# Optimization experiments

Hardware: AMD Instinct MI355X
Metric: run time of the kernel (lower is better)

## Reference

```python
import jax, jax.numpy as jnp
import numpy as np
from jax import lax

B, T = 32, 20
H, E, A, V = 256, 512, 256, 10000
GH, GW, D = 32, 32, 256          # info spatial grid and channel dim
P = GH * GW                      # num_pixels = 1024
IN_FLAT = P * D                  # 262144
REL = 128 * 128                  # 16384
LSTM_IN = E + D + H              # input to gate linears (x = [word, att_feat], then cat h)


def setup_inputs() -> dict:
    key = jax.random.key(0)
    ks = iter(jax.random.split(key, 40))
    def W(shape, scale=0.05):
        return jax.random.normal(next(ks), shape, jnp.float32) * scale
    inp = {}
    inp["info"] = jax.random.normal(next(ks), (B, GH, GW, D), jnp.float32)
    inp["relation"] = jax.random.normal(next(ks), (B, 128, 128), jnp.float32)
    inp["captions"] = jax.random.randint(next(ks), (B, T), 0, V)
    lens = jax.random.randint(next(ks), (B, 1), 5, T + 1).at[0, 0].set(T)
    inp["captions_lens"] = lens
    # embedding + attention
    inp["emb"] = W((V, E), 0.1)
    inp["W_enc"] = W((D, A)); inp["b_enc"] = jnp.zeros((A,), jnp.float32)
    inp["W_dec"] = W((H, A)); inp["b_dec"] = jnp.zeros((A,), jnp.float32)
    inp["W_full"] = W((A,));  inp["b_full"] = jnp.zeros((), jnp.float32)
    # MSLSTM cell (5 gate linears + mlp)
    for g in ("i", "f", "o", "g1", "g2"):
        inp[f"W_{g}"] = W((LSTM_IN, H)); inp[f"b_{g}"] = jnp.zeros((H,), jnp.float32)
    inp["W_mlp"] = W((2 * H, H)); inp["b_mlp"] = jnp.zeros((H,), jnp.float32)
    # f_beta, fc, init-state linears
    inp["W_beta"] = W((H, D)); inp["b_beta"] = jnp.zeros((D,), jnp.float32)
    inp["W_fc"] = W((H, V), 0.1); inp["b_fc"] = jnp.zeros((V,), jnp.float32)
    inp["W_ih"] = W((IN_FLAT, H), 0.005); inp["b_ih"] = jnp.zeros((H,), jnp.float32)
    inp["W_ic"] = W((IN_FLAT, H), 0.005); inp["b_ic"] = jnp.zeros((H,), jnp.float32)
    inp["W_iC"] = W((REL, H), 0.01);      inp["b_iC"] = jnp.zeros((H,), jnp.float32)
    return inp


def reference(info, relation, captions, captions_lens, emb,
              W_enc, b_enc, W_dec, b_dec, W_full, b_full,
              W_i, b_i, W_f, b_f, W_o, b_o, W_g1, b_g1, W_g2, b_g2,
              W_mlp, b_mlp, W_beta, b_beta, W_fc, b_fc,
              W_ih, b_ih, W_ic, b_ic, W_iC, b_iC):
    Bsz = captions.shape[0]
    info_f = info.reshape(Bsz, P, D)
    rel_f = relation.reshape(Bsz, REL)
    lens = captions_lens[:, 0]
    order = jnp.argsort(-lens)                      # sort descending by length
    lens = lens[order]
    caps = captions[order]
    info_f = info_f[order]
    rel_f = rel_f[order]
    sent_len = lens - 1
    Tm = captions.shape[1] - 1                      # static: max len forced to T in setup

    words = emb[caps]                               # (B, T, E)
    flat = info_f.reshape(Bsz, -1)                  # (B, P*D)
    h = flat @ W_ih + b_ih
    c = flat @ W_ic + b_ic
    C = rel_f @ W_iC + b_iC
    att1 = info_f @ W_enc + b_enc                   # (B, P, A) -- invariant over t

    def step(carry, xs):
        h, c, C = carry
        word, t = xs                                # word: (B, E)
        att2 = h @ W_dec + b_dec                    # (B, A)
        e = jax.nn.relu(att1 + att2[:, None, :]) @ W_full + b_full   # (B, P)
        alpha = jax.nn.softmax(e, axis=1)
        awf = jnp.einsum('bpd,bp->bd', info_f, alpha)                # (B, D)
        # note: gate=sigmoid(f_beta(h)) is computed in torch but its product is unused
        x = jnp.concatenate([word, awf, h], axis=1)  # cat([x, h]) with x=[word, awf]
        i = jax.nn.sigmoid(x @ W_i + b_i)
        f = jax.nn.sigmoid(x @ W_f + b_f)
        o = jax.nn.sigmoid(x @ W_o + b_o)
        g1 = jnp.tanh(x @ W_g1 + b_g1)
        g2 = jnp.tanh(x @ W_g2 + b_g2)
        new_c = f * c + i * g1
        new_C = f * C + i * g2
        new_h = o * jnp.tanh(jnp.concatenate([new_c, new_C], axis=1) @ W_mlp + b_mlp)
        pred = new_h @ W_fc + b_fc                  # dropout in eval mode = identity
        mask = (sent_len > t)[:, None].astype(pred.dtype)
        return (new_h, new_c, new_C), (pred * mask, alpha * mask)

    words_t = jnp.swapaxes(words[:, :Tm], 0, 1)     # (Tm, B, E)
    (_, (preds, alphas)) = lax.scan(step, (h, c, C), (words_t, jnp.arange(Tm)))
    predictions = jnp.swapaxes(preds, 0, 1)         # (B, Tm, V)
    alphas = jnp.swapaxes(alphas, 0, 1)             # (B, Tm, P)
    return predictions, alphas, order
```

## Files before the change

kernel.cpp:

```cpp
#include <hip/hip_runtime.h>
#include <math.h>

#define Bz 32
#define Tz 20
#define TMz 19
#define Vz 10000
#define INFLAT 262144
#define RELSZ 16384
#define NBLK 512

#define WS_PH     0
#define WS_PC     4194304
#define WS_ATT1H  0
#define WS_INFOH  4194304
#define WS_EXPE   8388608
#define WS_ZPART  8421376
#define WS_AWF    8421888
#define WS_GSP    8430080
#define WS_HST    8593920
#define WS_CST0   8602112
#define WS_CSTB0  8610304
#define WS_CST1   8618496
#define WS_CSTB1  8626688
#define WS_AT2P   8634880
#define WS_INTS   8700416
#define WS_PCHC   8701440

__device__ __forceinline__ float sigm(float x) { return 1.0f / (1.0f + expf(-x)); }

__device__ __forceinline__ unsigned short f2bf(float f) {
    unsigned int x = __float_as_uint(f);
    unsigned int r = (x + 0x7fffu + ((x >> 16) & 1u)) >> 16;
    return (unsigned short)r;
}

__device__ __forceinline__ float agload(const float* p) {
    return __hip_atomic_load(p, __ATOMIC_RELAXED, __HIP_MEMORY_SCOPE_AGENT);
}
__device__ __forceinline__ void agstore(float* p, float v) {
    __hip_atomic_store(p, v, __ATOMIC_RELAXED, __HIP_MEMORY_SCOPE_AGENT);
}
__device__ __forceinline__ int agloadi(const int* p) {
    return __hip_atomic_load(p, __ATOMIC_RELAXED, __HIP_MEMORY_SCOPE_AGENT);
}
__device__ __forceinline__ void agstorei(int* p, int v) {
    __hip_atomic_store(p, v, __ATOMIC_RELAXED, __HIP_MEMORY_SCOPE_AGENT);
}
__device__ __forceinline__ void agadd(float* p, float v) {
    __hip_atomic_fetch_add(p, v, __ATOMIC_RELAXED, __HIP_MEMORY_SCOPE_AGENT);
}

__device__ __forceinline__ void gl_lds16(const float* g, float* l) {
    __builtin_amdgcn_global_load_lds(
        (const __attribute__((address_space(1))) unsigned int*)g,
        (__attribute__((address_space(3))) unsigned int*)l,
        16, 0, 0);
}

__device__ __forceinline__ void gbar(int* slots, int* root, int gen) {
    asm volatile("s_waitcnt vmcnt(0)" ::: "memory");
    __syncthreads();
    if (blockIdx.x == 0) {
        int i0 = threadIdx.x, i1 = threadIdx.x + 256;
        if (i0 != 0) {
            while (agloadi(&slots[i0]) < gen) __builtin_amdgcn_s_sleep(1);
        }
        while (agloadi(&slots[i1]) < gen) __builtin_amdgcn_s_sleep(1);
        __syncthreads();
        if (threadIdx.x == 0) agstorei(root, gen);
    } else if (threadIdx.x == 0) {
        agstorei(&slots[blockIdx.x], gen);
        while (agloadi(root) < gen) __builtin_amdgcn_s_sleep(2);
    }
    __syncthreads();
    asm volatile("" ::: "memory");
}

__global__ void k_sort(const int* __restrict__ lens, float* __restrict__ out_order,
                       int* __restrict__ ord, int* __restrict__ sentlen, int* __restrict__ barmem) {
    if (threadIdx.x == 0 && blockIdx.x == 0) {
        for (int i = 0; i < 64 + NBLK; ++i) barmem[i] = 0;
        int l[Bz]; bool used[Bz];
        for (int b = 0; b < Bz; ++b) { l[b] = lens[b]; used[b] = false; }
        for (int i = 0; i < Bz; ++i) {
            int best = -1;
            for (int j = 0; j < Bz; ++j)
                if (!used[j] && (best < 0 || l[j] > l[best])) best = j;
            used[best] = true;
            ord[i] = best;
            sentlen[i] = l[best] - 1;
            out_order[i] = (float)best;
        }
    }
}

__global__ __launch_bounds__(256) void k_gemv2(const float* __restrict__ X, const int* __restrict__ ord,
                                               const float* __restrict__ W1, const float* __restrict__ W2,
                                               float* __restrict__ p1, float* __restrict__ p2) {
    __shared__ __align__(16) float wlds[8192];
    __shared__ __align__(16) float xsT[256 * 36];
    __shared__ int ords[32];
    int tid = threadIdx.x;
    int wv = tid >> 6, ln = tid & 63;
    size_t k0 = (size_t)blockIdx.x * 512;

    if (tid < 32) ords[tid] = ord[tid];
    __syncthreads();

    auto stage_xs = [&](int hh) {
        for (int idx = tid; idx < 2048; idx += 256) {
            int b = idx >> 6, kq = idx & 63;
            float4 v = *(const float4*)&X[(size_t)ords[b] * INFLAT + k0 + (size_t)hh * 256 + kq * 4];
            xsT[(kq * 4 + 0) * 36 + b] = v.x;
            xsT[(kq * 4 + 1) * 36 + b] = v.y;
            xsT[(kq * 4 + 2) * 36 + b] = v.z;
            xsT[(kq * 4 + 3) * 36 + b] = v.w;
        }
    };
    auto issue = [&](int n) {
        int slot = n & 1;
        size_t krow = k0 + (size_t)n * 8 + wv * 2;
        const float* g1 = W1 + krow * 256 + ln * 4;
        const float* g2 = W2 + krow * 256 + ln * 4;
        float* l1 = &wlds[slot * 4096 + (wv * 2) * 256 + ln * 4];
        float* l2 = &wlds[slot * 4096 + 2048 + (wv * 2) * 256 + ln * 4];
        gl_lds16(g1, l1);
        gl_lds16(g2, l2);
        gl_lds16(g1 + 256, l1 + 256);
        gl_lds16(g2 + 256, l2 + 256);
    };

    float ah[32], ac[32];
#pragma unroll
    for (int b = 0; b < 32; ++b) { ah[b] = 0.f; ac[b] = 0.f; }

    stage_xs(0);
    issue(0);

#pragma unroll 1
    for (int c = 0; c < 64; ++c) {
        if (c == 32) stage_xs(1);
        if (c + 1 < 64) {
            issue(c + 1);
            asm volatile("s_waitcnt vmcnt(4)" ::: "memory");
        } else {
            asm volatile("s_waitcnt vmcnt(0)" ::: "memory");
        }
        __syncthreads();
        int slot = c & 1;
        int xb0 = (c & 31) * 8;
#pragma unroll
        for (int kk = 0; kk < 8; ++kk) {
            float w1 = wlds[slot * 4096 + kk * 256 + tid];
            float w2 = wlds[slot * 4096 + 2048 + kk * 256 + tid];
            const float4* xr = (const float4*)&xsT[(xb0 + kk) * 36];
#pragma unroll
            for (int bq = 0; bq < 8; ++bq) {
                float4 x4 = xr[bq];
                ah[bq * 4 + 0] += x4.x * w1; ac[bq * 4 + 0] += x4.x * w2;
                ah[bq * 4 + 1] += x4.y * w1; ac[bq * 4 + 1] += x4.y * w2;
                ah[bq * 4 + 2] += x4.z * w1; ac[bq * 4 + 2] += x4.z * w2;
                ah[bq * 4 + 3] += x4.w * w1; ac[bq * 4 + 3] += x4.w * w2;
            }
        }
        __syncthreads();
    }
#pragma unroll
    for (int b = 0; b < 32; ++b) {
        size_t o = ((size_t)blockIdx.x * 32 + b) * 256 + tid;
        p1[o] = ah[b];
        p2[o] = ac[b];
    }
}

__global__ __launch_bounds__(256) void k_gemvC(const float* __restrict__ R, const int* __restrict__ ord,
                                               const float* __restrict__ W, float* __restrict__ p) {
    __shared__ float xs[32 * 128];
    __shared__ int ords[32];
    int tid = threadIdx.x, bx = blockIdx.x;
    if (tid < 32) ords[tid] = ord[tid];
    __syncthreads();
    int k0 = bx * 128;
    for (int idx = tid; idx < 32 * 128; idx += 256) {
        int b = idx >> 7, kk = idx & 127;
        xs[idx] = R[(size_t)ords[b] * RELSZ + k0 + kk];
    }
    __syncthreads();
    float acc[32];
#pragma unroll
    for (int b = 0; b < 32; ++b) acc[b] = 0.f;
    for (int kk = 0; kk < 128; ++kk) {
        float w = W[(size_t)(k0 + kk) * 256 + tid];
#pragma unroll
        for (int b = 0; b < 32; ++b) acc[b] += xs[b * 128 + kk] * w;
    }
#pragma unroll
    for (int b = 0; b < 32; ++b) p[((size_t)bx * 32 + b) * 256 + tid] = acc[b];
}

__global__ __launch_bounds__(256) void k_reduce3(const float* __restrict__ ph, const float* __restrict__ pc,
                                                 const float* __restrict__ pC,
                                                 const float* __restrict__ b_ih, const float* __restrict__ b_ic,
                                                 const float* __restrict__ b_iC,
                                                 float* __restrict__ hst, float* __restrict__ cst,
                                                 float* __restrict__ Cst) {
    int which = blockIdx.x >> 5, b = blockIdx.x & 31, j = threadIdx.x;
    if (which == 0) {
        float s0 = b_ih[j], s1 = 0.f, s2 = 0.f, s3 = 0.f;
        for (int c = 0; c < 512; c += 4) {
            s0 += ph[((size_t)((c + 0) * 32 + b)) * 256 + j];
            s1 += ph[((size_t)((c + 1) * 32 + b)) * 256 + j];
            s2 += ph[((size_t)((c + 2) * 32 + b)) * 256 + j];
            s3 += ph[((size_t)((c + 3) * 32 + b)) * 256 + j];
        }
        hst[b * 256 + j] = s0 + s1 + s2 + s3;
    } else if (which == 1) {
        float s0 = b_ic[j], s1 = 0.f, s2 = 0.f, s3 = 0.f;
        for (int c = 0; c < 512; c += 4) {
            s0 += pc[((size_t)((c + 0) * 32 + b)) * 256 + j];
            s1 += pc[((size_t)((c + 1) * 32 + b)) * 256 + j];
            s2 += pc[((size_t)((c + 2) * 32 + b)) * 256 + j];
            s3 += pc[((size_t)((c + 3) * 32 + b)) * 256 + j];
        }
        cst[b * 256 + j] = s0 + s1 + s2 + s3;
    } else {
        float s0 = b_iC[j], s1 = 0.f, s2 = 0.f, s3 = 0.f;
        for (int c = 0; c < 128; c += 4) {
            s0 += pC[((size_t)((c + 0) * 32 + b)) * 256 + j];
            s1 += pC[((size_t)((c + 1) * 32 + b)) * 256 + j];
            s2 += pC[((size_t)((c + 2) * 32 + b)) * 256 + j];
            s3 += pC[((size_t)((c + 3) * 32 + b)) * 256 + j];
        }
        Cst[b * 256 + j] = s0 + s1 + s2 + s3;
    }
}

__global__ __launch_bounds__(256) void k_init2(const float* __restrict__ hst, const float* __restrict__ W_dec,
                                               float* __restrict__ at2p, float* __restrict__ awf) {
    __shared__ __align__(16) float hs[8192];
    int tid = threadIdx.x;
    for (int i = blockIdx.x * 256 + tid; i < 8192; i += 1024) awf[i] = 0.f;
    for (int i = tid; i < 2048; i += 256) ((float4*)hs)[i] = ((const float4*)hst)[i];
    __syncthreads();
    int col = blockIdx.x * 64 + (tid & 63), bg = tid >> 6;
    float acc[8] = {0.f,0.f,0.f,0.f,0.f,0.f,0.f,0.f};
    for (int k = 0; k < 256; ++k) {
        float w = W_dec[(size_t)k * 256 + col];
#pragma unroll
        for (int bi = 0; bi < 8; ++bi) acc[bi] += hs[(bg * 8 + bi) * 256 + k] * w;
    }
#pragma unroll
    for (int bi = 0; bi < 8; ++bi) {
        int b = bg * 8 + bi;
        at2p[((size_t)(b * 8 + 0)) * 256 + col] = acc[bi];
#pragma unroll
        for (int ct = 1; ct < 8; ++ct) at2p[((size_t)(b * 8 + ct)) * 256 + col] = 0.f;
    }
}

__global__ __launch_bounds__(256) void k_att1(const float* __restrict__ info, const int* __restrict__ ord,
                                              const float* __restrict__ W, const float* __restrict__ bias,
                                              unsigned short* __restrict__ att1h,
                                              unsigned short* __restrict__ infoh) {
    __shared__ __align__(16) float xsT[256 * 36];
    int tid = threadIdx.x;
    int r0 = blockIdx.x * 32;
    int b = r0 >> 10, p0 = r0 & 1023;
    const float* src = info + (size_t)ord[b] * INFLAT + (size_t)p0 * 256;
    for (int idx = tid; idx < 2048; idx += 256) {
        int r = idx >> 6, kq = idx & 63;
        float4 v = *(const float4*)&src[r * 256 + kq * 4];
        xsT[(kq * 4 + 0) * 36 + r] = v.x;
        xsT[(kq * 4 + 1) * 36 + r] = v.y;
        xsT[(kq * 4 + 2) * 36 + r] = v.z;
        xsT[(kq * 4 + 3) * 36 + r] = v.w;
    }
    __syncthreads();
#pragma unroll 4
    for (int r = 0; r < 32; ++r)
        infoh[(size_t)(r0 + r) * 256 + tid] = f2bf(xsT[tid * 36 + r]);
    float acc[32];
#pragma unroll
    for (int r = 0; r < 32; ++r) acc[r] = 0.f;
    for (int k = 0; k < 256; ++k) {
        float w = W[k * 256 + tid];
        const float4* xr = (const float4*)&xsT[k * 36];
#pragma unroll
        for (int rq = 0; rq < 8; ++rq) {
            float4 x4 = xr[rq];
            acc[rq * 4 + 0] += x4.x * w;
            acc[rq * 4 + 1] += x4.y * w;
            acc[rq * 4 + 2] += x4.z * w;
            acc[rq * 4 + 3] += x4.w * w;
        }
    }
    float bj = bias[tid];
#pragma unroll
    for (int r = 0; r < 32; ++r)
        att1h[(size_t)(r0 + r) * 256 + tid] = f2bf(acc[r] + bj);
}

struct KArgs {
    const float *info, *emb, *W_dec, *b_dec, *W_full, *b_full;
    const float *W_i, *W_f, *W_o, *W_g1, *W_g2;
    const float *b_i, *b_f, *b_o, *b_g1, *b_g2;
    const float *W_mlp, *b_mlp, *W_fc, *b_fc;
    const int *caps;
    const unsigned short *att1h, *infoh;
    float *expe, *zpart, *awf, *gsp, *hst, *cst0, *Cst0, *cst1, *Cst1, *at2p;
    const int *ord, *slp;
    int *root, *slots;
    float *out_pred, *out_alpha;
};

__device__ void pred_task2(const KArgs& a, float* sm, int tile, int tm1) {
    int tid = threadIdx.x;
    for (int i = tid; i < 8192; i += 256) sm[i] = agload(&a.hst[i]);
    __syncthreads();
    int col = tile * 64 + (tid & 63), bg = tid >> 6;
    if (col >= Vz) return;
    float acc[8] = {0.f, 0.f, 0.f, 0.f, 0.f, 0.f, 0.f, 0.f};
    for (int jq = 0; jq < 64; ++jq) {
        float w0 = a.W_fc[(size_t)(jq * 4 + 0) * Vz + col];
        float w1 = a.W_fc[(size_t)(jq * 4 + 1) * Vz + col];
        float w2 = a.W_fc[(size_t)(jq * 4 + 2) * Vz + col];
        float w3 = a.W_fc[(size_t)(jq * 4 + 3) * Vz + col];
#pragma unroll
        for (int bi = 0; bi < 8; ++bi) {
            float4 h4 = *(const float4*)&sm[(bg * 8 + bi) * 256 + jq * 4];
            acc[bi] += h4.x * w0 + h4.y * w1 + h4.z * w2 + h4.w * w3;
        }
    }
    float bv = a.b_fc[col];
#pragma unroll
    for (int bi = 0; bi < 8; ++bi) {
        int b = bg * 8 + bi;
        float r = (a.slp[b] > tm1) ? (acc[bi] + bv) : 0.f;
        a.out_pred[((size_t)b * TMz + tm1) * Vz + col] = r;
    }
}

__global__ __launch_bounds__(256, 2) void k_steps(KArgs a) {
    __shared__ __align__(16) float sm[8224];
    __shared__ int caps_s[32];
    int bid = blockIdx.x, tid = threadIdx.x;
    int b = bid >> 4, sub = bid & 15;
    int gen = 0;

    for (int t = 0; t < TMz; ++t) {
        {
            float v = a.b_dec[tid];
#pragma unroll
            for (int ct = 0; ct < 8; ++ct) v += agload(&a.at2p[((size_t)(b * 8 + ct)) * 256 + tid]);
            sm[256 + tid] = v;
            sm[512 + tid] = a.W_full[tid];
            __syncthreads();
            int pl = tid & 63, kq = tid >> 6;
            const unsigned short* rowh = a.att1h + ((size_t)(b * 1024 + sub * 64 + pl)) * 256 + kq * 64;
            const float* a2 = sm + 256 + kq * 64;
            const float* wf = sm + 512 + kq * 64;
            float part = 0.f;
#pragma unroll
            for (int q = 0; q < 8; ++q) {
                uint4 u = ((const uint4*)rowh)[q];
                const float* A = a2 + q * 8;
                const float* W = wf + q * 8;
                part += fmaxf(__uint_as_float(u.x << 16)         + A[0], 0.f) * W[0];
                part += fmaxf(__uint_as_float(u.x & 0xffff0000u) + A[1], 0.f) * W[1];
                part += fmaxf(__uint_as_float(u.y << 16)         + A[2], 0.f) * W[2];
                part += fmaxf(__uint_as_float(u.y & 0xffff0000u) + A[3], 0.f) * W[3];
                part += fmaxf(__uint_as_float(u.z << 16)         + A[4], 0.f) * W[4];
                part += fmaxf(__uint_as_float(u.z & 0xffff0000u) + A[5], 0.f) * W[5];
                part += fmaxf(__uint_as_float(u.w << 16)         + A[6], 0.f) * W[6];
                part += fmaxf(__uint_as_float(u.w & 0xffff0000u) + A[7], 0.f) * W[7];
            }
            sm[768 + kq * 64 + pl] = part;
            __syncthreads();
            if (tid < 64) {
                float e = sm[768 + tid] + sm[832 + tid] + sm[896 + tid] + sm[960 + tid] + a.b_full[0];
                float ex = expf(e);
                agstore(&a.expe[b * 1024 + sub * 64 + tid], ex);
                sm[1024 + tid] = ex;
                float s = ex;
                s += __shfl_down(s, 32); s += __shfl_down(s, 16); s += __shfl_down(s, 8);
                s += __shfl_down(s, 4);  s += __shfl_down(s, 2);  s += __shfl_down(s, 1);
                if (tid == 0) agstore(&a.zpart[b * 16 + sub], s);
            }
            __syncthreads();
            int gg = tid >> 7, c2 = (tid & 127) * 2;
            const unsigned short* ibh = a.infoh + ((size_t)(b * 1024 + sub * 64 + gg)) * 256 + c2;
            const float* ex = sm + 1024;
            float a0 = 0.f, a1 = 0.f;
#pragma unroll
            for (int i = 0; i < 32; ++i) {
                unsigned int u = *(const unsigned int*)(ibh + (size_t)i * 512);
                float ev = ex[i * 2 + gg];
                a0 += ev * __uint_as_float(u << 16);
                a1 += ev * __uint_as_float(u & 0xffff0000u);
            }
            sm[1088 + gg * 256 + c2]     = a0;
            sm[1088 + gg * 256 + c2 + 1] = a1;
            __syncthreads();
            agadd(&a.awf[b * 256 + tid], sm[1088 + tid] + sm[1344 + tid]);
        }
        gbar(a.slots, a.root, ++gen);

        if (bid < 80) {
            int g = bid / 16, s16 = bid % 16;
            int ct = s16 >> 2, kc = s16 & 3;
            const float* Wg  = (g == 0) ? a.W_i : (g == 1) ? a.W_f : (g == 2) ? a.W_o : (g == 3) ? a.W_g1 : a.W_g2;
            if (kc == 2 && tid < 32) {
                float Z = 0.f;
#pragma unroll
                for (int c = 0; c < 16; ++c) Z += agload(&a.zpart[tid * 16 + c]);
                sm[8192 + tid] = 1.0f / Z;
            }
            if (kc < 2 && tid >= 64 && tid < 96) caps_s[tid - 64] = a.caps[a.ord[tid - 64] * Tz + t];
            __syncthreads();
            for (int idx = tid; idx < 8192; idx += 256) {
                int b2 = idx >> 8, kk = idx & 255;
                float v;
                if (kc == 0)      v = a.emb[(size_t)caps_s[b2] * 512 + kk];
                else if (kc == 1) v = a.emb[(size_t)caps_s[b2] * 512 + 256 + kk];
                else if (kc == 2) v = agload(&a.awf[b2 * 256 + kk]) * sm[8192 + b2];
                else              v = agload(&a.hst[b2 * 256 + kk]);
                sm[idx] = v;
            }
            __syncthreads();
            int col = ct * 64 + (tid & 63), bg = tid >> 6;
            float acc[8] = {0.f,0.f,0.f,0.f,0.f,0.f,0.f,0.f};
            int wbase = kc * 256;
            for (int kk = 0; kk < 256; kk += 4) {
                float w0 = Wg[(size_t)(wbase + kk + 0) * 256 + col];
                float w1 = Wg[(size_t)(wbase + kk + 1) * 256 + col];
                float w2 = Wg[(size_t)(wbase + kk + 2) * 256 + col];
                float w3 = Wg[(size_t)(wbase + kk + 3) * 256 + col];
#pragma unroll
                for (int bi = 0; bi < 8; ++bi) {
                    float4 x4 = *(const float4*)&sm[(bg * 8 + bi) * 256 + kk];
                    acc[bi] += x4.x * w0 + x4.y * w1 + x4.z * w2 + x4.w * w3;
                }
            }
#pragma unroll
            for (int bi = 0; bi < 8; ++bi)
                agstore(&a.gsp[((size_t)((g * 4 + kc) * 32 + bg * 8 + bi)) * 256 + col], acc[bi]);
        } else if (bid < 112) {
            int bb = bid - 80;
            float Z = 0.f;
#pragma unroll
            for (int c = 0; c < 16; ++c) Z += agload(&a.zpart[bb * 16 + c]);
            float invZ = 1.0f / Z;
            float am = (a.slp[bb] > t) ? invZ : 0.f;
            float* oal = a.out_alpha + ((size_t)bb * TMz + t) * 1024;
            for (int p = tid; p < 1024; p += 256) oal[p] = agload(&a.expe[bb * 1024 + p]) * am;
        } else if (t > 0 && bid < 269) {
            pred_task2(a, sm, bid - 112, t - 1);
        }
        gbar(a.slots, a.root, ++gen);

        if (bid < 256) {
            int bb = bid >> 3, ct = bid & 7;
            int j = tid;
            const float* csOld = (t & 1) ? a.cst1 : a.cst0;
            const float* CsOld = (t & 1) ? a.Cst1 : a.Cst0;
            float* csNew = (t & 1) ? a.cst0 : a.cst1;
            float* CsNew = (t & 1) ? a.Cst0 : a.Cst1;
            float gs[5];
#pragma unroll
            for (int g = 0; g < 5; ++g) {
                float s = 0.f;
#pragma unroll
                for (int kc = 0; kc < 4; ++kc)
                    s += agload(&a.gsp[((size_t)((g * 4 + kc) * 32 + bb)) * 256 + j]);
                gs[g] = s;
            }
            gs[0] += a.b_i[j]; gs[1] += a.b_f[j]; gs[2] += a.b_o[j];
            gs[3] += a.b_g1[j]; gs[4] += a.b_g2[j];
            float iv = sigm(gs[0]), fv = sigm(gs[1]), ov = sigm(gs[2]);
            float g1 = tanhf(gs[3]), g2 = tanhf(gs[4]);
            float nc = fv * agload(&csOld[bb * 256 + j]) + iv * g1;
            float nC = fv * agload(&CsOld[bb * 256 + j]) + iv * g2;
            if (ct == 0) {
                agstore(&csNew[bb * 256 + j], nc);
                agstore(&CsNew[bb * 256 + j], nC);
            }
            sm[j] = nc;
            sm[256 + j] = nC;
            sm[512 + j] = ov;
            __syncthreads();
            int colL = tid & 31, kth = tid >> 5;
            int col = ct * 32 + colL;
            float part = 0.f;
            const float* wm = a.W_mlp + col;
            for (int i = 0; i < 64; ++i) {
                int k = kth * 64 + i;
                part += sm[k] * wm[(size_t)k * 256];
            }
            sm[768 + colL * 9 + kth] = part;
            __syncthreads();
            if (tid < 32) {
                int c2 = ct * 32 + tid;
                float m = a.b_mlp[c2];
#pragma unroll
                for (int kk = 0; kk < 8; ++kk) m += sm[768 + tid * 9 + kk];
                float hv = sm[512 + c2] * tanhf(m);
                agstore(&a.hst[bb * 256 + c2], hv);
                sm[1056 + tid] = hv;
                agstore(&a.awf[bb * 256 + c2], 0.f);
            }
            __syncthreads();
            float acc = 0.f;
            const float* wd = a.W_dec + (size_t)(ct * 32) * 256 + tid;
#pragma unroll
            for (int kk = 0; kk < 32; ++kk) acc += sm[1056 + kk] * wd[(size_t)kk * 256];
            agstore(&a.at2p[((size_t)(bb * 8 + ct)) * 256 + tid], acc);
        }
        gbar(a.slots, a.root, ++gen);
    }

    if (bid >= 112 && bid < 269) pred_task2(a, sm, bid - 112, TMz - 1);
}

extern "C" void kernel_launch(void* const* d_in, const int* in_sizes, int n_in,
                              void* d_out, int out_size, void* d_ws, size_t ws_size,
                              hipStream_t stream) {
    const float* info  = (const float*)d_in[0];
    const float* rel   = (const float*)d_in[1];
    const int*   caps  = (const int*)d_in[2];
    const int*   lens  = (const int*)d_in[3];
    const float* emb   = (const float*)d_in[4];
    const float* W_enc = (const float*)d_in[5];
    const float* b_enc = (const float*)d_in[6];
    const float* W_dec = (const float*)d_in[7];
    const float* b_dec = (const float*)d_in[8];
    const float* W_full= (const float*)d_in[9];
    const float* b_full= (const float*)d_in[10];
    const float* W_i   = (const float*)d_in[11];
    const float* b_i   = (const float*)d_in[12];
    const float* W_f   = (const float*)d_in[13];
    const float* b_f   = (const float*)d_in[14];
    const float* W_o   = (const float*)d_in[15];
    const float* b_o   = (const float*)d_in[16];
    const float* W_g1  = (const float*)d_in[17];
    const float* b_g1  = (const float*)d_in[18];
    const float* W_g2  = (const float*)d_in[19];
    const float* b_g2  = (const float*)d_in[20];
    const float* W_mlp = (const float*)d_in[21];
    const float* b_mlp = (const float*)d_in[22];
    const float* W_fc  = (const float*)d_in[25];
    const float* b_fc  = (const float*)d_in[26];
    const float* W_ih  = (const float*)d_in[27];
    const float* b_ih  = (const float*)d_in[28];
    const float* W_ic  = (const float*)d_in[29];
    const float* b_ic  = (const float*)d_in[30];
    const float* W_iC  = (const float*)d_in[31];
    const float* b_iC  = (const float*)d_in[32];

    float* out = (float*)d_out;
    float* out_pred  = out;
    float* out_alpha = out + (size_t)Bz * TMz * Vz;
    float* out_order = out_alpha + (size_t)Bz * TMz * 1024;

    float* w = (float*)d_ws;
    float* ph   = w + WS_PH;
    float* pcp  = w + WS_PC;
    unsigned short* att1h = (unsigned short*)(w + WS_ATT1H);
    unsigned short* infoh = (unsigned short*)(w + WS_INFOH);
    float* expe = w + WS_EXPE;
    float* zpart= w + WS_ZPART;
    float* awf  = w + WS_AWF;
    float* gsp  = w + WS_GSP;
    float* hst  = w + WS_HST;
    float* cst0 = w + WS_CST0;
    float* Cst0 = w + WS_CSTB0;
    float* cst1 = w + WS_CST1;
    float* Cst1 = w + WS_CSTB1;
    float* at2p = w + WS_AT2P;
    int*   ordp = (int*)(w + WS_INTS);
    int*   slp  = ordp + 32;
    int*   barmem = ordp + 64;
    float* pC   = w + WS_PCHC;

    k_sort<<<1, 64, 0, stream>>>(lens, out_order, ordp, slp, barmem);
    k_gemv2<<<512, 256, 0, stream>>>(info, ordp, W_ih, W_ic, ph, pcp);
    k_gemvC<<<128, 256, 0, stream>>>(rel, ordp, W_iC, pC);
    k_reduce3<<<96, 256, 0, stream>>>(ph, pcp, pC, b_ih, b_ic, b_iC, hst, cst0, Cst0);
    k_init2<<<4, 256, 0, stream>>>(hst, W_dec, at2p, awf);
    k_att1<<<1024, 256, 0, stream>>>(info, ordp, W_enc, b_enc, att1h, infoh);

    KArgs ka;
    ka.info = info; ka.emb = emb; ka.W_dec = W_dec; ka.b_dec = b_dec;
    ka.W_full = W_full; ka.b_full = b_full;
    ka.W_i = W_i; ka.W_f = W_f; ka.W_o = W_o; ka.W_g1 = W_g1; ka.W_g2 = W_g2;
    ka.b_i = b_i; ka.b_f = b_f; ka.b_o = b_o; ka.b_g1 = b_g1; ka.b_g2 = b_g2;
    ka.W_mlp = W_mlp; ka.b_mlp = b_mlp; ka.W_fc = W_fc; ka.b_fc = b_fc;
    ka.caps = caps;
    ka.att1h = att1h; ka.infoh = infoh;
    ka.expe = expe; ka.zpart = zpart; ka.awf = awf;
    ka.gsp = gsp; ka.hst = hst;
    ka.cst0 = cst0; ka.Cst0 = Cst0; ka.cst1 = cst1; ka.Cst1 = Cst1;
    ka.at2p = at2p;
    ka.ord = ordp; ka.slp = slp;
    ka.root = barmem; ka.slots = barmem + 64;
    ka.out_pred = out_pred; ka.out_alpha = out_alpha;

    k_steps<<<NBLK, 256, 0, stream>>>(ka);
}
```

Baseline: 2.295 ms.

## Keep attention and info slices resident in LDS across steps; bf16 activations; atomic softmax sum

Each block of the persistent step kernel now loads its 64-row slices of att1h and infoh into LDS once, before the time loop, instead of re-reading them from global memory every step. The att1h slice is stored with an XOR swizzle to avoid bank conflicts. Gate-input and prediction activations are staged in LDS as bf16 rather than fp32. Per-block softmax partial sums are replaced by one atomic accumulator per batch row, and the 1/Z scaling is applied after the gate GEMV. This removes repeated global traffic for the attention tensors and trims the Z reduction. In exchange it needs 80 KB of LDS per block, which must still allow two blocks per CU for the cooperative grid, and bf16 activations lose precision.

```diff
diff --git a/kernel.cpp b/kernel.cpp
--- a/kernel.cpp
+++ b/kernel.cpp
@@ -14,7 +14,7 @@
 #define WS_ATT1H  0
 #define WS_INFOH  4194304
 #define WS_EXPE   8388608
-#define WS_ZPART  8421376
+#define WS_ZSUM   8421376
 #define WS_AWF    8421888
 #define WS_GSP    8430080
 #define WS_HST    8593920
@@ -33,6 +33,8 @@
     unsigned int r = (x + 0x7fffu + ((x >> 16) & 1u)) >> 16;
     return (unsigned short)r;
 }
+__device__ __forceinline__ float bfl(unsigned int u) { return __uint_as_float(u << 16); }
+__device__ __forceinline__ float bfh(unsigned int u) { return __uint_as_float(u & 0xffff0000u); }
 
 __device__ __forceinline__ float agload(const float* p) {
     return __hip_atomic_load(p, __ATOMIC_RELAXED, __HIP_MEMORY_SCOPE_AGENT);
@@ -236,10 +238,12 @@
 }
 
 __global__ __launch_bounds__(256) void k_init2(const float* __restrict__ hst, const float* __restrict__ W_dec,
-                                               float* __restrict__ at2p, float* __restrict__ awf) {
+                                               float* __restrict__ at2p, float* __restrict__ awf,
+                                               float* __restrict__ zsum) {
     __shared__ __align__(16) float hs[8192];
     int tid = threadIdx.x;
     for (int i = blockIdx.x * 256 + tid; i < 8192; i += 1024) awf[i] = 0.f;
+    if (blockIdx.x == 0 && tid < 32) zsum[tid] = 0.f;
     for (int i = tid; i < 2048; i += 256) ((float4*)hs)[i] = ((const float4*)hst)[i];
     __syncthreads();
     int col = blockIdx.x * 64 + (tid & 63), bg = tid >> 6;
@@ -307,15 +311,15 @@
     const float *W_mlp, *b_mlp, *W_fc, *b_fc;
     const int *caps;
     const unsigned short *att1h, *infoh;
-    float *expe, *zpart, *awf, *gsp, *hst, *cst0, *Cst0, *cst1, *Cst1, *at2p;
+    float *expe, *zsum, *awf, *gsp, *hst, *cst0, *Cst0, *cst1, *Cst1, *at2p;
     const int *ord, *slp;
     int *root, *slots;
     float *out_pred, *out_alpha;
 };
 
-__device__ void pred_task2(const KArgs& a, float* sm, int tile, int tm1) {
+__device__ void pred_task2(const KArgs& a, unsigned short* hb, int tile, int tm1) {
     int tid = threadIdx.x;
-    for (int i = tid; i < 8192; i += 256) sm[i] = agload(&a.hst[i]);
+    for (int i = tid; i < 8192; i += 256) hb[i] = f2bf(agload(&a.hst[i]));
     __syncthreads();
     int col = tile * 64 + (tid & 63), bg = tid >> 6;
     if (col >= Vz) return;
@@ -327,8 +331,8 @@
         float w3 = a.W_fc[(size_t)(jq * 4 + 3) * Vz + col];
 #pragma unroll
         for (int bi = 0; bi < 8; ++bi) {
-            float4 h4 = *(const float4*)&sm[(bg * 8 + bi) * 256 + jq * 4];
-            acc[bi] += h4.x * w0 + h4.y * w1 + h4.z * w2 + h4.w * w3;
+            uint2 u = *(const uint2*)&hb[(bg * 8 + bi) * 256 + jq * 4];
+            acc[bi] += bfl(u.x) * w0 + bfh(u.x) * w1 + bfl(u.y) * w2 + bfh(u.y) * w3;
         }
     }
     float bv = a.b_fc[col];
@@ -341,90 +345,104 @@
 }
 
 __global__ __launch_bounds__(256, 2) void k_steps(KArgs a) {
-    __shared__ __align__(16) float sm[8224];
-    __shared__ int caps_s[32];
+    __shared__ __align__(16) unsigned char smem[81920];
+    unsigned char* attB = smem;
+    unsigned char* infB = smem + 32768;
+    float* F = (float*)(smem + 65536);
+    unsigned short* S16 = (unsigned short*)(smem + 65536);
+
     int bid = blockIdx.x, tid = threadIdx.x;
     int b = bid >> 4, sub = bid & 15;
     int gen = 0;
 
+    {
+        const unsigned short* ag = a.att1h + (size_t)(b * 1024 + sub * 64) * 256;
+        const unsigned short* ig = a.infoh + (size_t)(b * 1024 + sub * 64) * 256;
+        for (int idx = tid; idx < 2048; idx += 256) {
+            int r = idx >> 5, qc = idx & 31;
+            uint4 v = *(const uint4*)(ag + (size_t)r * 256 + qc * 8);
+            *(uint4*)(attB + r * 512 + ((qc ^ (r & 7)) << 4)) = v;
+            uint4 w2 = *(const uint4*)(ig + (size_t)r * 256 + qc * 8);
+            *(uint4*)(infB + idx * 16) = w2;
+        }
+    }
+    __syncthreads();
+
     for (int t = 0; t < TMz; ++t) {
         {
             float v = a.b_dec[tid];
 #pragma unroll
             for (int ct = 0; ct < 8; ++ct) v += agload(&a.at2p[((size_t)(b * 8 + ct)) * 256 + tid]);
-            sm[256 + tid] = v;
-            sm[512 + tid] = a.W_full[tid];
+            F[tid] = v;
+            F[256 + tid] = a.W_full[tid];
             __syncthreads();
             int pl = tid & 63, kq = tid >> 6;
-            const unsigned short* rowh = a.att1h + ((size_t)(b * 1024 + sub * 64 + pl)) * 256 + kq * 64;
-            const float* a2 = sm + 256 + kq * 64;
-            const float* wf = sm + 512 + kq * 64;
             float part = 0.f;
 #pragma unroll
             for (int q = 0; q < 8; ++q) {
-                uint4 u = ((const uint4*)rowh)[q];
-                const float* A = a2 + q * 8;
-                const float* W = wf + q * 8;
-                part += fmaxf(__uint_as_float(u.x << 16)         + A[0], 0.f) * W[0];
-                part += fmaxf(__uint_as_float(u.x & 0xffff0000u) + A[1], 0.f) * W[1];
-                part += fmaxf(__uint_as_float(u.y << 16)         + A[2], 0.f) * W[2];
-                part += fmaxf(__uint_as_float(u.y & 0xffff0000u) + A[3], 0.f) * W[3];
-                part += fmaxf(__uint_as_float(u.z << 16)         + A[4], 0.f) * W[4];
-                part += fmaxf(__uint_as_float(u.z & 0xffff0000u) + A[5], 0.f) * W[5];
-                part += fmaxf(__uint_as_float(u.w << 16)         + A[6], 0.f) * W[6];
-                part += fmaxf(__uint_as_float(u.w & 0xffff0000u) + A[7], 0.f) * W[7];
-            }
-            sm[768 + kq * 64 + pl] = part;
+                int c = kq * 8 + q;
+                uint4 u = *(const uint4*)(attB + pl * 512 + ((c ^ (pl & 7)) << 4));
+                const float* A = F + kq * 64 + q * 8;
+                const float* W = F + 256 + kq * 64 + q * 8;
+                part += fmaxf(bfl(u.x) + A[0], 0.f) * W[0];
+                part += fmaxf(bfh(u.x) + A[1], 0.f) * W[1];
+                part += fmaxf(bfl(u.y) + A[2], 0.f) * W[2];
+                part += fmaxf(bfh(u.y) + A[3], 0.f) * W[3];
+                part += fmaxf(bfl(u.z) + A[4], 0.f) * W[4];
+                part += fmaxf(bfh(u.z) + A[5], 0.f) * W[5];
+                part += fmaxf(bfl(u.w) + A[6], 0.f) * W[6];
+                part += fmaxf(bfh(u.w) + A[7], 0.f) * W[7];
+            }
+            F[512 + kq * 64 + pl] = part;
             __syncthreads();
             if (tid < 64) {
-                float e = sm[768 + tid] + sm[832 + tid] + sm[896 + tid] + sm[960 + tid] + a.b_full[0];
+                float e = F[512 + tid] + F[576 + tid] + F[640 + tid] + F[704 + tid] + a.b_full[0];
                 float ex = expf(e);
                 agstore(&a.expe[b * 1024 + sub * 64 + tid], ex);
-                sm[1024 + tid] = ex;
+                F[768 + tid] = ex;
                 float s = ex;
                 s += __shfl_down(s, 32); s += __shfl_down(s, 16); s += __shfl_down(s, 8);
                 s += __shfl_down(s, 4);  s += __shfl_down(s, 2);  s += __shfl_down(s, 1);
-                if (tid == 0) agstore(&a.zpart[b * 16 + sub], s);
-            }
-            __syncthreads();
-            int gg = tid >> 7, c2 = (tid & 127) * 2;
-            const unsigned short* ibh = a.infoh + ((size_t)(b * 1024 + sub * 64 + gg)) * 256 + c2;
-            const float* ex = sm + 1024;
+                if (tid == 0) agadd(&a.zsum[b], s);
+            }
+            __syncthreads();
+            int gg = tid >> 7, c2 = tid & 127;
+            const unsigned char* ib = infB + gg * 512 + c2 * 4;
+            const float* ex = F + 768;
             float a0 = 0.f, a1 = 0.f;
 #pragma unroll
             for (int i = 0; i < 32; ++i) {
-                unsigned int u = *(const unsigned int*)(ibh + (size_t)i * 512);
+                unsigned int u = *(const unsigned int*)(ib + i * 1024);
                 float ev = ex[i * 2 + gg];
-                a0 += ev * __uint_as_float(u << 16);
-                a1 += ev * __uint_as_float(u & 0xffff0000u);
-            }
-            sm[1088 + gg * 256 + c2]     = a0;
-            sm[1088 + gg * 256 + c2 + 1] = a1;
-            __syncthreads();
-            agadd(&a.awf[b * 256 + tid], sm[1088 + tid] + sm[1344 + tid]);
+                a0 += ev * bfl(u);
+                a1 += ev * bfh(u);
+            }
+            F[832 + gg * 256 + c2 * 2]     = a0;
+            F[832 + gg * 256 + c2 * 2 + 1] = a1;
+            __syncthreads();
+            agadd(&a.awf[b * 256 + tid], F[832 + tid] + F[1088 + tid]);
         }
         gbar(a.slots, a.root, ++gen);
 
         if (bid < 80) {
             int g = bid / 16, s16 = bid % 16;
             int ct = s16 >> 2, kc = s16 & 3;
-            const float* Wg  = (g == 0) ? a.W_i : (g == 1) ? a.W_f : (g == 2) ? a.W_o : (g == 3) ? a.W_g1 : a.W_g2;
-            if (kc == 2 && tid < 32) {
-                float Z = 0.f;
-#pragma unroll
-                for (int c = 0; c < 16; ++c) Z += agload(&a.zpart[tid * 16 + c]);
-                sm[8192 + tid] = 1.0f / Z;
-            }
-            if (kc < 2 && tid >= 64 && tid < 96) caps_s[tid - 64] = a.caps[a.ord[tid - 64] * Tz + t];
-            __syncthreads();
+            const float* Wg = (g == 0) ? a.W_i : (g == 1) ? a.W_f : (g == 2) ? a.W_o : (g == 3) ? a.W_g1 : a.W_g2;
             for (int idx = tid; idx < 8192; idx += 256) {
                 int b2 = idx >> 8, kk = idx & 255;
                 float v;
-                if (kc == 0)      v = a.emb[(size_t)caps_s[b2] * 512 + kk];
-                else if (kc == 1) v = a.emb[(size_t)caps_s[b2] * 512 + 256 + kk];
-                else if (kc == 2) v = agload(&a.awf[b2 * 256 + kk]) * sm[8192 + b2];
-                else              v = agload(&a.hst[b2 * 256 + kk]);
-                sm[idx] = v;
+                if (kc == 0) {
+                    int cap = a.caps[a.ord[b2] * Tz + t];
+                    v = a.emb[(size_t)cap * 512 + kk];
+                } else if (kc == 1) {
+                    int cap = a.caps[a.ord[b2] * Tz + t];
+                    v = a.emb[(size_t)cap * 512 + 256 + kk];
+                } else if (kc == 2) {
+                    v = agload(&a.awf[b2 * 256 + kk]);
+                } else {
+                    v = agload(&a.hst[b2 * 256 + kk]);
+                }
+                S16[idx] = f2bf(v);
             }
             __syncthreads();
             int col = ct * 64 + (tid & 63), bg = tid >> 6;
@@ -437,8 +455,15 @@
                 float w3 = Wg[(size_t)(wbase + kk + 3) * 256 + col];
 #pragma unroll
                 for (int bi = 0; bi < 8; ++bi) {
-                    float4 x4 = *(const float4*)&sm[(bg * 8 + bi) * 256 + kk];
-                    acc[bi] += x4.x * w0 + x4.y * w1 + x4.z * w2 + x4.w * w3;
+                    uint2 u = *(const uint2*)&S16[(bg * 8 + bi) * 256 + kk];
+                    acc[bi] += bfl(u.x) * w0 + bfh(u.x) * w1 + bfl(u.y) * w2 + bfh(u.y) * w3;
+                }
+            }
+            if (kc == 2) {
+#pragma unroll
+                for (int bi = 0; bi < 8; ++bi) {
+                    float Z = agload(&a.zsum[bg * 8 + bi]);
+                    acc[bi] *= (1.0f / Z);
                 }
             }
 #pragma unroll
@@ -446,15 +471,13 @@
                 agstore(&a.gsp[((size_t)((g * 4 + kc) * 32 + bg * 8 + bi)) * 256 + col], acc[bi]);
         } else if (bid < 112) {
             int bb = bid - 80;
-            float Z = 0.f;
-#pragma unroll
-            for (int c = 0; c < 16; ++c) Z += agload(&a.zpart[bb * 16 + c]);
+            float Z = agload(&a.zsum[bb]);
             float invZ = 1.0f / Z;
             float am = (a.slp[bb] > t) ? invZ : 0.f;
             float* oal = a.out_alpha + ((size_t)bb * TMz + t) * 1024;
             for (int p = tid; p < 1024; p += 256) oal[p] = agload(&a.expe[bb * 1024 + p]) * am;
         } else if (t > 0 && bid < 269) {
-            pred_task2(a, sm, bid - 112, t - 1);
+            pred_task2(a, S16, bid - 112, t - 1);
         }
         gbar(a.slots, a.root, ++gen);
 
@@ -484,9 +507,10 @@
                 agstore(&csNew[bb * 256 + j], nc);
                 agstore(&CsNew[bb * 256 + j], nC);
             }
-            sm[j] = nc;
-            sm[256 + j] = nC;
-            sm[512 + j] = ov;
+            if (ct == 1 && tid == 0) agstore(&a.zsum[bb], 0.f);
+            F[j] = nc;
+            F[256 + j] = nC;
+            F[512 + j] = ov;
             __syncthreads();
             int colL = tid & 31, kth = tid >> 5;
             int col = ct * 32 + colL;
@@ -494,31 +518,31 @@
             const float* wm = a.W_mlp + col;
             for (int i = 0; i < 64; ++i) {
                 int k = kth * 64 + i;
-                part += sm[k] * wm[(size_t)k * 256];
-            }
-            sm[768 + colL * 9 + kth] = part;
+                part += F[k] * wm[(size_t)k * 256];
+            }
+            F[768 + colL * 9 + kth] = part;
             __syncthreads();
             if (tid < 32) {
                 int c2 = ct * 32 + tid;
                 float m = a.b_mlp[c2];
 #pragma unroll
-                for (int kk = 0; kk < 8; ++kk) m += sm[768 + tid * 9 + kk];
-                float hv = sm[512 + c2] * tanhf(m);
+                for (int kk = 0; kk < 8; ++kk) m += F[768 + tid * 9 + kk];
+                float hv = F[512 + c2] * tanhf(m);
                 agstore(&a.hst[bb * 256 + c2], hv);
-                sm[1056 + tid] = hv;
+                F[1056 + tid] = hv;
                 agstore(&a.awf[bb * 256 + c2], 0.f);
             }
             __syncthreads();
             float acc = 0.f;
             const float* wd = a.W_dec + (size_t)(ct * 32) * 256 + tid;
 #pragma unroll
-            for (int kk = 0; kk < 32; ++kk) acc += sm[1056 + kk] * wd[(size_t)kk * 256];
+            for (int kk = 0; kk < 32; ++kk) acc += F[1056 + kk] * wd[(size_t)kk * 256];
             agstore(&a.at2p[((size_t)(bb * 8 + ct)) * 256 + tid], acc);
         }
         gbar(a.slots, a.root, ++gen);
     }
 
-    if (bid >= 112 && bid < 269) pred_task2(a, sm, bid - 112, TMz - 1);
+    if (bid >= 112 && bid < 269) pred_task2(a, S16, bid - 112, TMz - 1);
 }
 
 extern "C" void kernel_launch(void* const* d_in, const int* in_sizes, int n_in,
@@ -567,7 +591,7 @@
     unsigned short* att1h = (unsigned short*)(w + WS_ATT1H);
     unsigned short* infoh = (unsigned short*)(w + WS_INFOH);
     float* expe = w + WS_EXPE;
-    float* zpart= w + WS_ZPART;
+    float* zsum = w + WS_ZSUM;
     float* awf  = w + WS_AWF;
     float* gsp  = w + WS_GSP;
     float* hst  = w + WS_HST;
@@ -585,7 +609,7 @@
     k_gemv2<<<512, 256, 0, stream>>>(info, ordp, W_ih, W_ic, ph, pcp);
     k_gemvC<<<128, 256, 0, stream>>>(rel, ordp, W_iC, pC);
     k_reduce3<<<96, 256, 0, stream>>>(ph, pcp, pC, b_ih, b_ic, b_iC, hst, cst0, Cst0);
-    k_init2<<<4, 256, 0, stream>>>(hst, W_dec, at2p, awf);
+    k_init2<<<4, 256, 0, stream>>>(hst, W_dec, at2p, awf, zsum);
     k_att1<<<1024, 256, 0, stream>>>(info, ordp, W_enc, b_enc, att1h, infoh);
 
     KArgs ka;
@@ -596,7 +620,7 @@
     ka.W_mlp = W_mlp; ka.b_mlp = b_mlp; ka.W_fc = W_fc; ka.b_fc = b_fc;
     ka.caps = caps;
     ka.att1h = att1h; ka.infoh = infoh;
-    ka.expe = expe; ka.zpart = zpart; ka.awf = awf;
+    ka.expe = expe; ka.zsum = zsum; ka.awf = awf;
     ka.gsp = gsp; ka.hst = hst;
     ka.cst0 = cst0; ka.Cst0 = Cst0; ka.cst1 = cst1; ka.Cst1 = Cst1;
     ka.at2p = at2p;
```

Result: faster. 2.183 ms (-4.9%).
